# Optimization experiments

Measured on AMD Instinct MI355X. Metric: run time of the kernel, lower is better.

Reference implementation:

```python
import jax, jax.numpy as jnp
import numpy as np

B, S, E = 2, 2048, 2048
H, W = 16, 256  # num_heads, window_size
D = E // H      # head_dim = 128


def setup_inputs() -> dict:
    key = jax.random.key(0)
    ks = jax.random.split(key, 9)
    s = 1.0 / np.sqrt(E)
    return {
        "x": jax.random.normal(ks[0], (B, S, E), dtype=jnp.float32),
        "Wq": jax.random.normal(ks[1], (E, E), dtype=jnp.float32) * s,
        "bq": jax.random.normal(ks[2], (E,), dtype=jnp.float32) * 0.01,
        "Wk": jax.random.normal(ks[3], (E, E), dtype=jnp.float32) * s,
        "bk": jax.random.normal(ks[4], (E,), dtype=jnp.float32) * 0.01,
        "Wv": jax.random.normal(ks[5], (E, E), dtype=jnp.float32) * s,
        "bv": jax.random.normal(ks[6], (E,), dtype=jnp.float32) * 0.01,
        "Wo": jax.random.normal(ks[7], (E, E), dtype=jnp.float32) * s,
        "bo": jax.random.normal(ks[8], (E,), dtype=jnp.float32) * 0.01,
    }


def reference(x, Wq, bq, Wk, bk, Wv, bv, Wo, bo):
    Bsz, Sl, _ = x.shape
    # projections -> [B, H, S, D]
    def proj(Wt, bt):
        return (x @ Wt + bt).reshape(Bsz, Sl, H, D).transpose(0, 2, 1, 3)
    q = proj(Wq, bq)
    k = proj(Wk, bk)
    v = proj(Wv, bv)
    # scores [B, H, S, S]
    scores = jnp.einsum("bhqd,bhkd->bhqk", q, k) / jnp.sqrt(jnp.float32(D))
    # causal sliding-window mask: q_pos - W < k_pos <= q_pos
    q_pos = jnp.arange(Sl)[:, None]
    k_pos = jnp.arange(Sl)[None, :]
    valid = (k_pos <= q_pos) & (k_pos > q_pos - W)
    scores = jnp.where(valid, scores, jnp.float32(-jnp.inf))
    attn = jax.nn.softmax(scores, axis=-1)
    ctx = jnp.einsum("bhqk,bhkd->bhqd", attn, v)
    ctx = ctx.transpose(0, 2, 1, 3).reshape(Bsz, Sl, E)
    out = ctx @ Wo + bo
    return out, k, v
```

## Files before the change

kernel.cpp:

```cpp
#include <hip/hip_runtime.h>
#include <hip/hip_bf16.h>

#define SEQ 2048
#define EMB 2048
#define NH 16
#define WIN 256
#define HD 128
#define KDIM 2048
#define NDIM 2048

typedef __bf16 bf16x8 __attribute__((ext_vector_type(8)));
typedef float f32x4 __attribute__((ext_vector_type(4)));

__device__ __forceinline__ ushort f2bf(float f) {
  unsigned int x = __float_as_uint(f);
  unsigned int r = (x + 0x7fffu + ((x >> 16) & 1u)) >> 16;
  return (ushort)r;
}

__device__ __forceinline__ void gl16(const ushort* g, ushort* l) {
  __builtin_amdgcn_global_load_lds(
      (const __attribute__((address_space(1))) ushort*)g,
      (__attribute__((address_space(3))) ushort*)l, 16, 0, 0);
}

__global__ __launch_bounds__(256) void xconv_kernel(
    const float* __restrict__ x, ushort* __restrict__ xb) {
  size_t i = ((size_t)blockIdx.x * 256 + threadIdx.x) * 8;
  float4 f0 = *(const float4*)&x[i];
  float4 f1 = *(const float4*)&x[i + 4];
  union { ushort u[8]; uint4 v; } pk;
  pk.u[0] = f2bf(f0.x); pk.u[1] = f2bf(f0.y);
  pk.u[2] = f2bf(f0.z); pk.u[3] = f2bf(f0.w);
  pk.u[4] = f2bf(f1.x); pk.u[5] = f2bf(f1.y);
  pk.u[6] = f2bf(f1.z); pk.u[7] = f2bf(f1.w);
  *(uint4*)&xb[i] = pk.v;
}

__global__ __launch_bounds__(256) void wtrans_kernel(
    const float* __restrict__ w0, const float* __restrict__ w1,
    const float* __restrict__ w2, const float* __restrict__ w3,
    ushort* __restrict__ wt) {
  __shared__ __align__(16) float tf[64 * 132];
  const int t = threadIdx.x;
  const int nblk = blockIdx.x, kblk = blockIdx.y, mat = blockIdx.z;
  const float* Wp = mat == 0 ? w0 : mat == 1 ? w1 : mat == 2 ? w2 : w3;
  const int n0 = nblk * 128, k0 = kblk * 64;
#pragma unroll
  for (int p = 0; p < 8; ++p) {
    int idx = p * 256 + t;
    int kk = idx >> 5;
    int nn = (idx & 31) * 4;
    float4 v = *(const float4*)&Wp[(size_t)(k0 + kk) * NDIM + n0 + nn];
    *(float4*)&tf[kk * 132 + nn] = v;
  }
  __syncthreads();
  ushort* dst = wt + (size_t)mat * ((size_t)NDIM * KDIM) +
                (size_t)(nblk * 32 + kblk) * 8192;
#pragma unroll
  for (int p = 0; p < 4; ++p) {
    int s = p * 256 + t;
    int r = s >> 3, kc = s & 7;
    int cg = kc ^ (r & 7);
    union { ushort u[8]; uint4 v; } pk;
#pragma unroll
    for (int j = 0; j < 8; ++j) pk.u[j] = f2bf(tf[(cg * 8 + j) * 132 + r]);
    *(uint4*)&dst[s * 8] = pk.v;
  }
}

template <int MODE>
__global__ __launch_bounds__(512, 2) void gemm_kernel(
    const ushort* __restrict__ Ab, const ushort* __restrict__ Wt,
    const float* __restrict__ b0, const float* __restrict__ b1,
    const float* __restrict__ b2, float* __restrict__ outF,
    ushort* __restrict__ outQ) {
  __shared__ __align__(16) ushort L[3 * 24576];
  const int t = threadIdx.x;
  const int w = t >> 6, lane = t & 63;
  const int l15 = lane & 15, lg = lane >> 4;
  const int wm = w >> 1, wn = w & 1;
  const int bid = blockIdx.x + (blockIdx.y << 4);
  const int wkid = (bid & 7) * 32 + (bid >> 3);
  const int mblk = wkid & 15, nblk = wkid >> 4;
  const int z = blockIdx.z;
  const int m0 = mblk * 256, n0 = nblk * 128;
  const ushort* wz = Wt + (size_t)z * ((size_t)NDIM * KDIM) +
                     (size_t)nblk * 32 * 8192;

  const ushort* aS[4];
#pragma unroll
  for (int j = 0; j < 4; ++j) {
    int s = j * 512 + t;
    int r = s >> 3, kc = s & 7;
    int cg = kc ^ (r & 7);
    aS[j] = Ab + (size_t)(m0 + r) * KDIM + cg * 8;
  }
  const ushort* bS[2];
#pragma unroll
  for (int j = 0; j < 2; ++j) bS[j] = wz + (size_t)(j * 512 + t) * 8;

  f32x4 acc[4][4] = {};

#define STAGE(ts, p)                                                     \
  {                                                                      \
    ushort* Ad = &L[(p) * 24576 + w * 512];                              \
    ushort* Bd = &L[(p) * 24576 + 16384 + w * 512];                      \
    size_t ko = (size_t)(ts) * 64;                                       \
    size_t bo = (size_t)(ts) * 8192;                                     \
    gl16(aS[0] + ko, Ad);                                                \
    gl16(aS[1] + ko, Ad + 4096);                                         \
    gl16(aS[2] + ko, Ad + 8192);                                         \
    gl16(aS[3] + ko, Ad + 12288);                                        \
    gl16(bS[0] + bo, Bd);                                                \
    gl16(bS[1] + bo, Bd + 4096);                                         \
  }

  const int NT = KDIM / 64;
  STAGE(0, 0)
  STAGE(1, 1)

  for (int tk = 0; tk < NT; ++tk) {
    asm volatile("s_waitcnt vmcnt(6)\n\ts_barrier" ::: "memory");
    const int ts = (tk + 2 < NT) ? (tk + 2) : (NT - 1);
    const int sp = (tk + 2) % 3;
    STAGE(ts, sp)
    const ushort* Ar = &L[(tk % 3) * 24576];
    const ushort* Br = Ar + 16384;

#pragma unroll
    for (int kk = 0; kk < 2; ++kk) {
      bf16x8 af[4], bfn[2];
#pragma unroll
      for (int mi = 0; mi < 4; ++mi) {
        int row = wm * 64 + mi * 16 + l15;
        af[mi] = *(const bf16x8*)&Ar[row * 64 + (((kk * 4 + lg) ^ (row & 7)) * 8)];
      }
#pragma unroll
      for (int ni = 0; ni < 2; ++ni) {
        int nr = wn * 64 + ni * 16 + l15;
        bfn[ni] = *(const bf16x8*)&Br[nr * 64 + (((kk * 4 + lg) ^ (nr & 7)) * 8)];
      }
      __builtin_amdgcn_s_barrier();
      __builtin_amdgcn_s_setprio(1);
#pragma unroll
      for (int mi = 0; mi < 4; ++mi)
#pragma unroll
        for (int ni = 0; ni < 2; ++ni)
          acc[mi][ni] = __builtin_amdgcn_mfma_f32_16x16x32_bf16(
              af[mi], bfn[ni], acc[mi][ni], 0, 0, 0);
      __builtin_amdgcn_s_setprio(0);
      bf16x8 bf2[2];
#pragma unroll
      for (int ni = 0; ni < 2; ++ni) {
        int nr = wn * 64 + (ni + 2) * 16 + l15;
        bf2[ni] = *(const bf16x8*)&Br[nr * 64 + (((kk * 4 + lg) ^ (nr & 7)) * 8)];
      }
      __builtin_amdgcn_s_barrier();
      __builtin_amdgcn_s_setprio(1);
#pragma unroll
      for (int mi = 0; mi < 4; ++mi)
#pragma unroll
        for (int ni = 0; ni < 2; ++ni)
          acc[mi][ni + 2] = __builtin_amdgcn_mfma_f32_16x16x32_bf16(
              af[mi], bf2[ni], acc[mi][ni + 2], 0, 0, 0);
      __builtin_amdgcn_s_setprio(0);
    }
  }
#undef STAGE

  const float* bias = (MODE == 0) ? b0 : (z == 0 ? b0 : z == 1 ? b1 : b2);
#pragma unroll
  for (int ni = 0; ni < 4; ++ni) {
    int nl = wn * 64 + ni * 16 + l15;
    int n = n0 + nl;
    float bv = bias[n];
#pragma unroll
    for (int mi = 0; mi < 4; ++mi) {
#pragma unroll
      for (int r = 0; r < 4; ++r) {
        int m = m0 + wm * 64 + mi * 16 + lg * 4 + r;
        float val = acc[mi][ni][r] + bv;
        if (MODE == 0) {
          outF[(size_t)m * NDIM + n] = val;
        } else {
          int b = m >> 11, s = m & 2047;
          size_t idx = (((size_t)b * NH + nblk) * SEQ + s) * HD + nl;
          if (z == 0) outQ[idx] = f2bf(val);
          else outF[(z == 1 ? (size_t)8388608u : (size_t)16777216u) + idx] = val;
        }
      }
    }
  }
}

__global__ __launch_bounds__(256) void attn_kernel(
    const ushort* __restrict__ Qb, const float* __restrict__ Kf,
    const float* __restrict__ Vf, ushort* __restrict__ ctx) {
  __shared__ __align__(16) ushort Kl[64 * 128];
  __shared__ __align__(16) ushort Vl[128 * 72];
  __shared__ __align__(16) ushort Pl[4 * 16 * 72];
  const int t = threadIdx.x;
  const int bh = blockIdx.x;
  const int q0 = blockIdx.y * 64;
  const int lane = t & 63, w = t >> 6;
  const int l15 = lane & 15, lg = lane >> 4;
  const int b = bh >> 4, h = bh & 15;
  const ushort* Qbase = Qb + (size_t)bh * SEQ * HD;
  const float* Kbase = Kf + (size_t)bh * SEQ * HD;
  const float* Vbase = Vf + (size_t)bh * SEQ * HD;

  bf16x8 aq[4];
#pragma unroll
  for (int ds = 0; ds < 4; ++ds)
    aq[ds] = *(const bf16x8*)&Qbase[(size_t)(q0 + w * 16 + l15) * HD + ds * 32 + lg * 8];

  f32x4 accc[8] = {};
  float mrow[4], lrow[4];
#pragma unroll
  for (int r = 0; r < 4; ++r) { mrow[r] = -1e30f; lrow[r] = 0.f; }

  int ktlo = (q0 - WIN + 1) >> 6;
  if (ktlo < 0) ktlo = 0;
  const int kthi = q0 >> 6;

  for (int kt = ktlo; kt <= kthi; ++kt) {
    __syncthreads();
#pragma unroll
    for (int p = 0; p < 4; ++p) {
      int idx = p * 256 + t;
      int row = idx >> 4, cs = idx & 15;
      int c = cs ^ (row & 7);
      const float* sp = &Kbase[(size_t)(kt * 64 + row) * HD + c * 8];
      float4 f0 = *(const float4*)sp;
      float4 f1 = *(const float4*)(sp + 4);
      union { ushort u[8]; uint4 v; } pk;
      pk.u[0] = f2bf(f0.x); pk.u[1] = f2bf(f0.y);
      pk.u[2] = f2bf(f0.z); pk.u[3] = f2bf(f0.w);
      pk.u[4] = f2bf(f1.x); pk.u[5] = f2bf(f1.y);
      pk.u[6] = f2bf(f1.z); pk.u[7] = f2bf(f1.w);
      *(uint4*)&Kl[row * 128 + cs * 8] = pk.v;
    }
#pragma unroll
    for (int p = 0; p < 4; ++p) {
      int idx = p * 256 + t;
      int key = idx & 63, dc = idx >> 6;
      const float* sp = &Vbase[(size_t)(kt * 64 + key) * HD + dc * 8];
      float4 f0 = *(const float4*)sp;
      float4 f1 = *(const float4*)(sp + 4);
      Vl[(dc * 8 + 0) * 72 + key] = f2bf(f0.x);
      Vl[(dc * 8 + 1) * 72 + key] = f2bf(f0.y);
      Vl[(dc * 8 + 2) * 72 + key] = f2bf(f0.z);
      Vl[(dc * 8 + 3) * 72 + key] = f2bf(f0.w);
      Vl[(dc * 8 + 4) * 72 + key] = f2bf(f1.x);
      Vl[(dc * 8 + 5) * 72 + key] = f2bf(f1.y);
      Vl[(dc * 8 + 6) * 72 + key] = f2bf(f1.z);
      Vl[(dc * 8 + 7) * 72 + key] = f2bf(f1.w);
    }
    __syncthreads();

    f32x4 sacc[4] = {};
#pragma unroll
    for (int ds = 0; ds < 4; ++ds) {
#pragma unroll
      for (int kf = 0; kf < 4; ++kf) {
        int key = kf * 16 + l15;
        bf16x8 kb = *(const bf16x8*)&Kl[key * 128 + (((ds * 4 + lg) ^ (key & 7)) * 8)];
        sacc[kf] = __builtin_amdgcn_mfma_f32_16x16x32_bf16(aq[ds], kb, sacc[kf], 0, 0, 0);
      }
    }

    const float scale = 0.08838834764831845f;
    const float L2E = 1.4426950408889634f;
#pragma unroll
    for (int r = 0; r < 4; ++r) {
      int q = q0 + w * 16 + lg * 4 + r;
      float sv[4];
      float mx = -1e30f;
#pragma unroll
      for (int kf = 0; kf < 4; ++kf) {
        int key = kt * 64 + kf * 16 + l15;
        float s = sacc[kf][r] * scale;
        bool valid = (key <= q) && (key + WIN > q);
        s = valid ? s : -1e30f;
        sv[kf] = s;
        mx = fmaxf(mx, s);
      }
      mx = fmaxf(mx, __shfl_xor(mx, 1));
      mx = fmaxf(mx, __shfl_xor(mx, 2));
      mx = fmaxf(mx, __shfl_xor(mx, 4));
      mx = fmaxf(mx, __shfl_xor(mx, 8));
      float mnew = fmaxf(mrow[r], mx);
      float sf = exp2f((mrow[r] - mnew) * L2E);
      float ps = 0.f;
#pragma unroll
      for (int kf = 0; kf < 4; ++kf) {
        float p = (sv[kf] > -1e29f) ? exp2f((sv[kf] - mnew) * L2E) : 0.f;
        ps += p;
        Pl[w * 1152 + (lg * 4 + r) * 72 + kf * 16 + l15] = f2bf(p);
      }
      ps += __shfl_xor(ps, 1);
      ps += __shfl_xor(ps, 2);
      ps += __shfl_xor(ps, 4);
      ps += __shfl_xor(ps, 8);
      lrow[r] = lrow[r] * sf + ps;
      mrow[r] = mnew;
#pragma unroll
      for (int nf = 0; nf < 8; ++nf) accc[nf][r] *= sf;
    }

#pragma unroll
    for (int ks = 0; ks < 2; ++ks) {
      bf16x8 pa = *(const bf16x8*)&Pl[w * 1152 + l15 * 72 + ks * 32 + lg * 8];
#pragma unroll
      for (int nf = 0; nf < 8; ++nf) {
        bf16x8 vb = *(const bf16x8*)&Vl[(nf * 16 + l15) * 72 + ks * 32 + lg * 8];
        accc[nf] = __builtin_amdgcn_mfma_f32_16x16x32_bf16(pa, vb, accc[nf], 0, 0, 0);
      }
    }
  }

#pragma unroll
  for (int r = 0; r < 4; ++r) {
    int q = q0 + w * 16 + lg * 4 + r;
    float inv = 1.0f / lrow[r];
    size_t rowoff = ((size_t)b * SEQ + q) * EMB + (size_t)h * HD;
#pragma unroll
    for (int nf = 0; nf < 8; ++nf)
      ctx[rowoff + nf * 16 + l15] = f2bf(accc[nf][r] * inv);
  }
}

extern "C" void kernel_launch(void* const* d_in, const int* in_sizes, int n_in,
                              void* d_out, int out_size, void* d_ws, size_t ws_size,
                              hipStream_t stream) {
  const float* x  = (const float*)d_in[0];
  const float* Wq = (const float*)d_in[1];
  const float* bq = (const float*)d_in[2];
  const float* Wk = (const float*)d_in[3];
  const float* bk = (const float*)d_in[4];
  const float* Wv = (const float*)d_in[5];
  const float* bv = (const float*)d_in[6];
  const float* Wo = (const float*)d_in[7];
  const float* bo = (const float*)d_in[8];
  float* out = (float*)d_out;
  ushort* ws = (ushort*)d_ws;
  ushort* Wt   = ws;
  ushort* Qb   = ws + 16777216;
  ushort* xb   = ws + 25165824;
  ushort* ctxb = xb;

  xconv_kernel<<<4096, 256, 0, stream>>>(x, xb);
  wtrans_kernel<<<dim3(16, 32, 4), 256, 0, stream>>>(Wq, Wk, Wv, Wo, Wt);
  gemm_kernel<1><<<dim3(16, 16, 3), 512, 0, stream>>>(xb, Wt, bq, bk, bv, out, Qb);
  attn_kernel<<<dim3(32, 32), 256, 0, stream>>>(Qb, out + 8388608, out + 16777216, ctxb);
  gemm_kernel<0><<<dim3(16, 16, 1), 512, 0, stream>>>(ctxb, Wt + (size_t)3 * 4194304,
                                                      bo, nullptr, nullptr, out, nullptr);
}
```

Baseline: 238.6 us.

## Split GEMM into 256x256-tile QKV kernel and double-buffered output-projection kernel

The templated GEMM is replaced by two kernels. The QKV projection now uses 256x256 output tiles over a flattened 6144-wide N dimension, with a 4x2 wave layout, double-buffered LDS, and interleaved load/MFMA phases. This raises arithmetic intensity per tile and cuts the block count. The output projection moves from triple to double buffering, with loads issued after the compute. The trade-offs are more accumulator registers per wave and a shallower prefetch depth, which could hurt occupancy or expose memory latency.

```diff
diff --git a/kernel.cpp b/kernel.cpp
--- a/kernel.cpp
+++ b/kernel.cpp
@@ -23,6 +23,10 @@
       (const __attribute__((address_space(1))) ushort*)g,
       (__attribute__((address_space(3))) ushort*)l, 16, 0, 0);
 }
+
+#define MFMA __builtin_amdgcn_mfma_f32_16x16x32_bf16
+#define BAR __builtin_amdgcn_s_barrier
+#define PRIO __builtin_amdgcn_s_setprio
 
 __global__ __launch_bounds__(256) void xconv_kernel(
     const float* __restrict__ x, ushort* __restrict__ xb) {
@@ -43,20 +47,18 @@
     ushort* __restrict__ wt) {
   __shared__ __align__(16) float tf[64 * 132];
   const int t = threadIdx.x;
-  const int nblk = blockIdx.x, kblk = blockIdx.y, mat = blockIdx.z;
+  const int nb = blockIdx.x, kblk = blockIdx.y, mat = blockIdx.z;
   const float* Wp = mat == 0 ? w0 : mat == 1 ? w1 : mat == 2 ? w2 : w3;
-  const int n0 = nblk * 128, k0 = kblk * 64;
+  const int n0 = nb * 128, k0 = kblk * 64;
 #pragma unroll
   for (int p = 0; p < 8; ++p) {
-    int idx = p * 256 + t;
-    int kk = idx >> 5;
-    int nn = (idx & 31) * 4;
+    int kk = (t >> 5) + 8 * p;
+    int nn = (t & 31) * 4;
     float4 v = *(const float4*)&Wp[(size_t)(k0 + kk) * NDIM + n0 + nn];
     *(float4*)&tf[kk * 132 + nn] = v;
   }
   __syncthreads();
-  ushort* dst = wt + (size_t)mat * ((size_t)NDIM * KDIM) +
-                (size_t)(nblk * 32 + kblk) * 8192;
+  ushort* dst = wt + (size_t)((mat * 16 + nb) * 32 + kblk) * 8192;
 #pragma unroll
   for (int p = 0; p < 4; ++p) {
     int s = p * 256 + t;
@@ -69,126 +71,248 @@
   }
 }
 
-template <int MODE>
-__global__ __launch_bounds__(512, 2) void gemm_kernel(
+__global__ __launch_bounds__(512, 2) void gemm_qkv_kernel(
     const ushort* __restrict__ Ab, const ushort* __restrict__ Wt,
-    const float* __restrict__ b0, const float* __restrict__ b1,
-    const float* __restrict__ b2, float* __restrict__ outF,
+    const float* __restrict__ bq, const float* __restrict__ bk,
+    const float* __restrict__ bv, float* __restrict__ outF,
     ushort* __restrict__ outQ) {
-  __shared__ __align__(16) ushort L[3 * 24576];
+  __shared__ __align__(16) ushort L[65536];
+  const int t = threadIdx.x;
+  const int w = t >> 6, lane = t & 63;
+  const int l15 = lane & 15, lg = lane >> 4;
+  const int wm = w >> 2, wn = w & 3;
+  const int bid = blockIdx.x;
+  const int wkid = (bid & 7) * 48 + (bid >> 3);
+  const int mblk = wkid & 15, nb = wkid >> 4;
+  const int m0 = mblk * 256;
+  const ushort* wbase = Wt + (size_t)nb * 524288;
+
+  const ushort* aS[4];
+#pragma unroll
+  for (int j = 0; j < 4; ++j) {
+    int s = j * 512 + t;
+    int r = s >> 3, kc = s & 7;
+    aS[j] = Ab + (size_t)(m0 + r) * KDIM + (kc ^ (r & 7)) * 8;
+  }
+  const ushort* bS[4];
+  bS[0] = wbase + (size_t)t * 8;
+  bS[1] = wbase + (size_t)(t + 512) * 8;
+  bS[2] = wbase + 262144 + (size_t)t * 8;
+  bS[3] = wbase + 262144 + (size_t)(t + 512) * 8;
+
+  f32x4 acc[8][4] = {};
+
+#define STAGE_A(kt, buf)                                        \
+  { ushort* d = &L[(buf) * 16384 + w * 512];                    \
+    gl16(aS[0] + (kt) * 64, d);                                 \
+    gl16(aS[1] + (kt) * 64, d + 4096);                          \
+    gl16(aS[2] + (kt) * 64, d + 8192);                          \
+    gl16(aS[3] + (kt) * 64, d + 12288); }
+#define STAGE_B(kt, buf)                                        \
+  { ushort* d = &L[32768 + (buf) * 16384 + w * 512];            \
+    gl16(bS[0] + (kt) * 8192, d);                               \
+    gl16(bS[1] + (kt) * 8192, d + 4096);                        \
+    gl16(bS[2] + (kt) * 8192, d + 8192);                        \
+    gl16(bS[3] + (kt) * 8192, d + 12288); }
+
+  const int NT = 32;
+  STAGE_A(0, 0) STAGE_B(0, 0) STAGE_A(1, 1) STAGE_B(1, 1)
+  asm volatile("s_waitcnt vmcnt(8)" ::: "memory");
+  BAR();
+
+  for (int tk = 0; tk < NT; ++tk) {
+    const int buf = tk & 1;
+    const int ts = (tk + 2 < NT) ? tk + 2 : NT - 1;
+    const ushort* Ar = &L[buf * 16384];
+    const ushort* Br = &L[32768 + buf * 16384];
+    bf16x8 a0[8], a1[8], bb[4];
+#pragma unroll
+    for (int mi = 0; mi < 8; ++mi) {
+      int row = wm * 128 + mi * 16 + l15;
+      a0[mi] = *(const bf16x8*)&Ar[row * 64 + ((lg ^ (row & 7)) * 8)];
+    }
+    {
+      int r0 = wn * 64 + l15, r1 = r0 + 16;
+      bb[0] = *(const bf16x8*)&Br[r0 * 64 + ((lg ^ (r0 & 7)) * 8)];
+      bb[1] = *(const bf16x8*)&Br[r1 * 64 + ((lg ^ (r1 & 7)) * 8)];
+    }
+    BAR(); PRIO(1);
+#pragma unroll
+    for (int mi = 0; mi < 8; ++mi) acc[mi][0] = MFMA(a0[mi], bb[0], acc[mi][0], 0, 0, 0);
+#pragma unroll
+    for (int mi = 0; mi < 8; ++mi) acc[mi][1] = MFMA(a0[mi], bb[1], acc[mi][1], 0, 0, 0);
+    PRIO(0); BAR();
+    {
+      int r2 = wn * 64 + 32 + l15, r3 = r2 + 16;
+      bb[2] = *(const bf16x8*)&Br[r2 * 64 + ((lg ^ (r2 & 7)) * 8)];
+      bb[3] = *(const bf16x8*)&Br[r3 * 64 + ((lg ^ (r3 & 7)) * 8)];
+    }
+#pragma unroll
+    for (int mi = 0; mi < 8; ++mi) {
+      int row = wm * 128 + mi * 16 + l15;
+      a1[mi] = *(const bf16x8*)&Ar[row * 64 + (((4 + lg) ^ (row & 7)) * 8)];
+    }
+    BAR(); PRIO(1);
+#pragma unroll
+    for (int mi = 0; mi < 8; ++mi) acc[mi][2] = MFMA(a0[mi], bb[2], acc[mi][2], 0, 0, 0);
+#pragma unroll
+    for (int mi = 0; mi < 8; ++mi) acc[mi][3] = MFMA(a0[mi], bb[3], acc[mi][3], 0, 0, 0);
+    PRIO(0); BAR();
+    {
+      int r0 = wn * 64 + l15, r1 = r0 + 16;
+      bb[0] = *(const bf16x8*)&Br[r0 * 64 + (((4 + lg) ^ (r0 & 7)) * 8)];
+      bb[1] = *(const bf16x8*)&Br[r1 * 64 + (((4 + lg) ^ (r1 & 7)) * 8)];
+    }
+    STAGE_A(ts, buf)
+    BAR(); PRIO(1);
+#pragma unroll
+    for (int mi = 0; mi < 8; ++mi) acc[mi][0] = MFMA(a1[mi], bb[0], acc[mi][0], 0, 0, 0);
+#pragma unroll
+    for (int mi = 0; mi < 8; ++mi) acc[mi][1] = MFMA(a1[mi], bb[1], acc[mi][1], 0, 0, 0);
+    PRIO(0); BAR();
+    {
+      int r2 = wn * 64 + 32 + l15, r3 = r2 + 16;
+      bb[2] = *(const bf16x8*)&Br[r2 * 64 + (((4 + lg) ^ (r2 & 7)) * 8)];
+      bb[3] = *(const bf16x8*)&Br[r3 * 64 + (((4 + lg) ^ (r3 & 7)) * 8)];
+    }
+    STAGE_B(ts, buf)
+    BAR(); PRIO(1);
+#pragma unroll
+    for (int mi = 0; mi < 8; ++mi) acc[mi][2] = MFMA(a1[mi], bb[2], acc[mi][2], 0, 0, 0);
+#pragma unroll
+    for (int mi = 0; mi < 8; ++mi) acc[mi][3] = MFMA(a1[mi], bb[3], acc[mi][3], 0, 0, 0);
+    PRIO(0);
+    asm volatile("s_waitcnt vmcnt(8)" ::: "memory");
+    BAR();
+  }
+#undef STAGE_A
+#undef STAGE_B
+
+  const int z = nb >> 3;
+  const float* bias = z == 0 ? bq : z == 1 ? bk : bv;
+#pragma unroll
+  for (int ni = 0; ni < 4; ++ni) {
+    int nl = wn * 64 + ni * 16 + l15;
+    int n6 = (nb & 7) * 256 + nl;
+    float bvv = bias[n6];
+    int h = n6 >> 7, d = n6 & 127;
+#pragma unroll
+    for (int mi = 0; mi < 8; ++mi) {
+#pragma unroll
+      for (int r = 0; r < 4; ++r) {
+        int m = m0 + wm * 128 + mi * 16 + lg * 4 + r;
+        float val = acc[mi][ni][r] + bvv;
+        int b = m >> 11, s = m & 2047;
+        size_t idx = (((size_t)b * NH + h) * SEQ + s) * HD + d;
+        if (z == 0) outQ[idx] = f2bf(val);
+        else if (z == 1) outF[(size_t)8388608u + idx] = val;
+        else outF[(size_t)16777216u + idx] = val;
+      }
+    }
+  }
+}
+
+__global__ __launch_bounds__(512, 2) void gemm_out_kernel(
+    const ushort* __restrict__ Ab, const ushort* __restrict__ Wt,
+    const float* __restrict__ bo, float* __restrict__ outF) {
+  __shared__ __align__(16) ushort L[49152];
   const int t = threadIdx.x;
   const int w = t >> 6, lane = t & 63;
   const int l15 = lane & 15, lg = lane >> 4;
   const int wm = w >> 1, wn = w & 1;
-  const int bid = blockIdx.x + (blockIdx.y << 4);
+  const int bid = blockIdx.x;
   const int wkid = (bid & 7) * 32 + (bid >> 3);
-  const int mblk = wkid & 15, nblk = wkid >> 4;
-  const int z = blockIdx.z;
-  const int m0 = mblk * 256, n0 = nblk * 128;
-  const ushort* wz = Wt + (size_t)z * ((size_t)NDIM * KDIM) +
-                     (size_t)nblk * 32 * 8192;
+  const int mblk = wkid & 15, nb = wkid >> 4;
+  const int m0 = mblk * 256;
+  const ushort* wbase = Wt + (size_t)(48 + nb) * 262144;
 
   const ushort* aS[4];
 #pragma unroll
   for (int j = 0; j < 4; ++j) {
     int s = j * 512 + t;
     int r = s >> 3, kc = s & 7;
-    int cg = kc ^ (r & 7);
-    aS[j] = Ab + (size_t)(m0 + r) * KDIM + cg * 8;
+    aS[j] = Ab + (size_t)(m0 + r) * KDIM + (kc ^ (r & 7)) * 8;
   }
   const ushort* bS[2];
-#pragma unroll
-  for (int j = 0; j < 2; ++j) bS[j] = wz + (size_t)(j * 512 + t) * 8;
+  bS[0] = wbase + (size_t)t * 8;
+  bS[1] = wbase + (size_t)(t + 512) * 8;
 
   f32x4 acc[4][4] = {};
 
-#define STAGE(ts, p)                                                     \
-  {                                                                      \
-    ushort* Ad = &L[(p) * 24576 + w * 512];                              \
-    ushort* Bd = &L[(p) * 24576 + 16384 + w * 512];                      \
-    size_t ko = (size_t)(ts) * 64;                                       \
-    size_t bo = (size_t)(ts) * 8192;                                     \
-    gl16(aS[0] + ko, Ad);                                                \
-    gl16(aS[1] + ko, Ad + 4096);                                         \
-    gl16(aS[2] + ko, Ad + 8192);                                         \
-    gl16(aS[3] + ko, Ad + 12288);                                        \
-    gl16(bS[0] + bo, Bd);                                                \
-    gl16(bS[1] + bo, Bd + 4096);                                         \
-  }
-
-  const int NT = KDIM / 64;
-  STAGE(0, 0)
-  STAGE(1, 1)
+#define STAGE_A(kt, buf)                                        \
+  { ushort* d = &L[(buf) * 16384 + w * 512];                    \
+    gl16(aS[0] + (kt) * 64, d);                                 \
+    gl16(aS[1] + (kt) * 64, d + 4096);                          \
+    gl16(aS[2] + (kt) * 64, d + 8192);                          \
+    gl16(aS[3] + (kt) * 64, d + 12288); }
+#define STAGE_B(kt, buf)                                        \
+  { ushort* d = &L[32768 + (buf) * 8192 + w * 512];             \
+    gl16(bS[0] + (kt) * 8192, d);                               \
+    gl16(bS[1] + (kt) * 8192, d + 4096); }
+
+  const int NT = 32;
+  STAGE_A(0, 0) STAGE_B(0, 0) STAGE_A(1, 1) STAGE_B(1, 1)
+  asm volatile("s_waitcnt vmcnt(6)" ::: "memory");
+  BAR();
 
   for (int tk = 0; tk < NT; ++tk) {
-    asm volatile("s_waitcnt vmcnt(6)\n\ts_barrier" ::: "memory");
-    const int ts = (tk + 2 < NT) ? (tk + 2) : (NT - 1);
-    const int sp = (tk + 2) % 3;
-    STAGE(ts, sp)
-    const ushort* Ar = &L[(tk % 3) * 24576];
-    const ushort* Br = Ar + 16384;
-
-#pragma unroll
-    for (int kk = 0; kk < 2; ++kk) {
-      bf16x8 af[4], bfn[2];
-#pragma unroll
-      for (int mi = 0; mi < 4; ++mi) {
-        int row = wm * 64 + mi * 16 + l15;
-        af[mi] = *(const bf16x8*)&Ar[row * 64 + (((kk * 4 + lg) ^ (row & 7)) * 8)];
-      }
-#pragma unroll
-      for (int ni = 0; ni < 2; ++ni) {
-        int nr = wn * 64 + ni * 16 + l15;
-        bfn[ni] = *(const bf16x8*)&Br[nr * 64 + (((kk * 4 + lg) ^ (nr & 7)) * 8)];
-      }
-      __builtin_amdgcn_s_barrier();
-      __builtin_amdgcn_s_setprio(1);
-#pragma unroll
-      for (int mi = 0; mi < 4; ++mi)
-#pragma unroll
-        for (int ni = 0; ni < 2; ++ni)
-          acc[mi][ni] = __builtin_amdgcn_mfma_f32_16x16x32_bf16(
-              af[mi], bfn[ni], acc[mi][ni], 0, 0, 0);
-      __builtin_amdgcn_s_setprio(0);
-      bf16x8 bf2[2];
-#pragma unroll
-      for (int ni = 0; ni < 2; ++ni) {
-        int nr = wn * 64 + (ni + 2) * 16 + l15;
-        bf2[ni] = *(const bf16x8*)&Br[nr * 64 + (((kk * 4 + lg) ^ (nr & 7)) * 8)];
-      }
-      __builtin_amdgcn_s_barrier();
-      __builtin_amdgcn_s_setprio(1);
-#pragma unroll
-      for (int mi = 0; mi < 4; ++mi)
-#pragma unroll
-        for (int ni = 0; ni < 2; ++ni)
-          acc[mi][ni + 2] = __builtin_amdgcn_mfma_f32_16x16x32_bf16(
-              af[mi], bf2[ni], acc[mi][ni + 2], 0, 0, 0);
-      __builtin_amdgcn_s_setprio(0);
-    }
-  }
-#undef STAGE
-
-  const float* bias = (MODE == 0) ? b0 : (z == 0 ? b0 : z == 1 ? b1 : b2);
+    const int buf = tk & 1;
+    const int ts = (tk + 2 < NT) ? tk + 2 : NT - 1;
+    const ushort* Ar = &L[buf * 16384];
+    const ushort* Br = &L[32768 + buf * 8192];
+    bf16x8 af[4], bf[4];
+#pragma unroll
+    for (int mi = 0; mi < 4; ++mi) {
+      int row = wm * 64 + mi * 16 + l15;
+      af[mi] = *(const bf16x8*)&Ar[row * 64 + ((lg ^ (row & 7)) * 8)];
+    }
+#pragma unroll
+    for (int ni = 0; ni < 4; ++ni) {
+      int row = wn * 64 + ni * 16 + l15;
+      bf[ni] = *(const bf16x8*)&Br[row * 64 + ((lg ^ (row & 7)) * 8)];
+    }
+    BAR(); PRIO(1);
+#pragma unroll
+    for (int mi = 0; mi < 4; ++mi)
+#pragma unroll
+      for (int ni = 0; ni < 4; ++ni)
+        acc[mi][ni] = MFMA(af[mi], bf[ni], acc[mi][ni], 0, 0, 0);
+    PRIO(0); BAR();
+#pragma unroll
+    for (int mi = 0; mi < 4; ++mi) {
+      int row = wm * 64 + mi * 16 + l15;
+      af[mi] = *(const bf16x8*)&Ar[row * 64 + (((4 + lg) ^ (row & 7)) * 8)];
+    }
+#pragma unroll
+    for (int ni = 0; ni < 4; ++ni) {
+      int row = wn * 64 + ni * 16 + l15;
+      bf[ni] = *(const bf16x8*)&Br[row * 64 + (((4 + lg) ^ (row & 7)) * 8)];
+    }
+    BAR(); PRIO(1);
+#pragma unroll
+    for (int mi = 0; mi < 4; ++mi)
+#pragma unroll
+      for (int ni = 0; ni < 4; ++ni)
+        acc[mi][ni] = MFMA(af[mi], bf[ni], acc[mi][ni], 0, 0, 0);
+    PRIO(0);
+    STAGE_A(ts, buf)
+    STAGE_B(ts, buf)
+    asm volatile("s_waitcnt vmcnt(6)" ::: "memory");
+    BAR();
+  }
+#undef STAGE_A
+#undef STAGE_B
+
 #pragma unroll
   for (int ni = 0; ni < 4; ++ni) {
-    int nl = wn * 64 + ni * 16 + l15;
-    int n = n0 + nl;
-    float bv = bias[n];
+    int n = nb * 128 + wn * 64 + ni * 16 + l15;
+    float bvv = bo[n];
 #pragma unroll
     for (int mi = 0; mi < 4; ++mi) {
 #pragma unroll
       for (int r = 0; r < 4; ++r) {
         int m = m0 + wm * 64 + mi * 16 + lg * 4 + r;
-        float val = acc[mi][ni][r] + bv;
-        if (MODE == 0) {
-          outF[(size_t)m * NDIM + n] = val;
-        } else {
-          int b = m >> 11, s = m & 2047;
-          size_t idx = (((size_t)b * NH + nblk) * SEQ + s) * HD + nl;
-          if (z == 0) outQ[idx] = f2bf(val);
-          else outF[(z == 1 ? (size_t)8388608u : (size_t)16777216u) + idx] = val;
-        }
+        outF[(size_t)m * NDIM + n] = acc[mi][ni][r] + bvv;
       }
     }
   }
@@ -266,7 +390,7 @@
       for (int kf = 0; kf < 4; ++kf) {
         int key = kf * 16 + l15;
         bf16x8 kb = *(const bf16x8*)&Kl[key * 128 + (((ds * 4 + lg) ^ (key & 7)) * 8)];
-        sacc[kf] = __builtin_amdgcn_mfma_f32_16x16x32_bf16(aq[ds], kb, sacc[kf], 0, 0, 0);
+        sacc[kf] = MFMA(aq[ds], kb, sacc[kf], 0, 0, 0);
       }
     }
 
@@ -315,7 +439,7 @@
 #pragma unroll
       for (int nf = 0; nf < 8; ++nf) {
         bf16x8 vb = *(const bf16x8*)&Vl[(nf * 16 + l15) * 72 + ks * 32 + lg * 8];
-        accc[nf] = __builtin_amdgcn_mfma_f32_16x16x32_bf16(pa, vb, accc[nf], 0, 0, 0);
+        accc[nf] = MFMA(pa, vb, accc[nf], 0, 0, 0);
       }
     }
   }
@@ -352,8 +476,7 @@
 
   xconv_kernel<<<4096, 256, 0, stream>>>(x, xb);
   wtrans_kernel<<<dim3(16, 32, 4), 256, 0, stream>>>(Wq, Wk, Wv, Wo, Wt);
-  gemm_kernel<1><<<dim3(16, 16, 3), 512, 0, stream>>>(xb, Wt, bq, bk, bv, out, Qb);
+  gemm_qkv_kernel<<<384, 512, 0, stream>>>(xb, Wt, bq, bk, bv, out, Qb);
   attn_kernel<<<dim3(32, 32), 256, 0, stream>>>(Qb, out + 8388608, out + 16777216, ctxb);
-  gemm_kernel<0><<<dim3(16, 16, 1), 512, 0, stream>>>(ctxb, Wt + (size_t)3 * 4194304,
-                                                      bo, nullptr, nullptr, out, nullptr);
-}
+  gemm_out_kernel<<<256, 512, 0, stream>>>(ctxb, Wt, bo, out);
+}
```

New measurement: 253.3 us. 6.2% more time.
